# Kernel optimization log

Hardware: AMD Instinct MI355X
Metric: run time of the kernel (lower is better)

The kernel has to match this reference:

```python
import jax, jax.numpy as jnp
import numpy as np
import math

B, NB, HID, KD, NH = 256, 16, 512, 64, 8

def setup_inputs() -> dict:
    key = jax.random.key(0)
    ks = jax.random.split(key, 6)
    s = lambda fan_in: 1.0 / math.sqrt(fan_in)
    return {
        "h": jax.random.normal(ks[0], (B, NB, HID), dtype=jnp.float32),
        "mask": jax.random.randint(ks[1], (B, NB), 0, 2, dtype=jnp.int32),
        "Wk": jax.random.normal(ks[2], (NB, HID, KD * NH), dtype=jnp.float32) * s(HID),
        "Wq": jax.random.normal(ks[3], (NB, HID, KD * NH), dtype=jnp.float32) * s(HID),
        "Wv": jax.random.normal(ks[4], (NB, HID, HID * NH), dtype=jnp.float32) * s(HID),
        "Wo": jax.random.normal(ks[5], (NB, HID * NH, HID), dtype=jnp.float32) * s(HID * NH),
    }

def _group_linear(x, w):
    # x: (B, NB, din), w: (NB, din, dout) -> (B, NB, dout)
    return jnp.einsum('bnd,nde->bne', x, w)

def reference(h, mask, Wk, Wq, Wv, Wo):
    # grouped QKV projections
    k = _group_linear(h, Wk).reshape(B, NB, NH, KD).transpose(0, 2, 1, 3)    # (B,H,NB,KD)
    q = _group_linear(h, Wq).reshape(B, NB, NH, KD).transpose(0, 2, 1, 3)    # (B,H,NB,KD)
    v = _group_linear(h, Wv).reshape(B, NB, NH, HID).transpose(0, 2, 1, 3)   # (B,H,NB,HID)
    scores = jnp.einsum('bhqd,bhkd->bhqk', q, k) / math.sqrt(KD)             # (B,H,NB,NB)
    probs = jax.nn.softmax(scores, axis=-1)
    # post-softmax row mask: mask (B,NB) -> (B,1,NB,1)
    probs = probs * mask.astype(probs.dtype)[:, None, :, None]
    ctx = jnp.einsum('bhqk,bhkd->bhqd', probs, v)                            # (B,H,NB,HID)
    ctx = ctx.transpose(0, 2, 1, 3).reshape(B, NB, NH * HID)                 # (B,NB,H*HID)
    return _group_linear(ctx, Wo)                                            # (B,NB,HID)
```

## Files before the change

kernel.cpp:

```cpp
#include <hip/hip_runtime.h>


typedef short s16x4 __attribute__((ext_vector_type(4)));
typedef short s16x8 __attribute__((ext_vector_type(8)));
typedef float f32x4 __attribute__((ext_vector_type(4)));

__device__ __forceinline__ unsigned short f2bf(float f) {
  unsigned int u = __builtin_bit_cast(unsigned int, f);
  u += 0x7fffu + ((u >> 16) & 1u);
  return (unsigned short)(u >> 16);
}
__device__ __forceinline__ float bf2f(unsigned short s) {
  unsigned int u = ((unsigned int)s) << 16;
  return __builtin_bit_cast(float, u);
}

__global__ __launch_bounds__(256) void cvt_h(const float* __restrict__ h,
                                             unsigned short* __restrict__ hb)
{
  int i = (blockIdx.x * 256 + threadIdx.x) * 4;
  float4 v = *reinterpret_cast<const float4*>(h + i);
  s16x4 st = { (short)f2bf(v.x), (short)f2bf(v.y), (short)f2bf(v.z), (short)f2bf(v.w) };
  *reinterpret_cast<s16x4*>(hb + i) = st;
}

__global__ __launch_bounds__(256) void qkv_gemm(
    const unsigned short* __restrict__ hb, const float* __restrict__ Wq,
    const float* __restrict__ Wk, const float* __restrict__ Wv,
    unsigned short* __restrict__ qo, unsigned short* __restrict__ ko,
    unsigned short* __restrict__ vo)
{
  const int g    = blockIdx.y;
  const int n0   = blockIdx.x * 64;
  const int tid  = threadIdx.x;
  const int lane = tid & 63;
  const int wave = tid >> 6;
  const int wm   = wave * 64;

  const float* W; unsigned short* out; size_t obase; int oldc, wN, c0;
  if (n0 < 512)       { W = Wq + (size_t)g * 262144;  out = qo; obase = (size_t)g * 512;  oldc = 8192;  wN = 512;  c0 = n0; }
  else if (n0 < 1024) { W = Wk + (size_t)g * 262144;  out = ko; obase = (size_t)g * 512;  oldc = 8192;  wN = 512;  c0 = n0 - 512; }
  else                { W = Wv + (size_t)g * 2097152; out = vo; obase = (size_t)g * 4096; oldc = 65536; wN = 4096; c0 = n0 - 1024; }

  const unsigned short* A = hb + (size_t)g * 512;

  __shared__ unsigned short As[256][32];
  __shared__ unsigned short Bs[64][36];

  f32x4 acc[4][4];
  #pragma unroll
  for (int i = 0; i < 4; i++)
    #pragma unroll
    for (int j = 0; j < 4; j++) acc[i][j] = (f32x4){0.f, 0.f, 0.f, 0.f};

  const int fr = lane & 15, fq = lane >> 4;

  for (int k0 = 0; k0 < 512; k0 += 32) {
    __syncthreads();
    #pragma unroll
    for (int p = 0; p < 4; p++) {
      int idx = p * 256 + tid;
      int row = idx >> 2, kq = idx & 3;
      *reinterpret_cast<s16x8*>(&As[row][kq * 8]) =
          *reinterpret_cast<const s16x8*>(A + (size_t)row * 8192 + k0 + kq * 8);
    }
    #pragma unroll
    for (int p = 0; p < 2; p++) {
      int idx = p * 256 + tid;
      int n = idx & 63, kc = idx >> 6;
      const float* wp = W + (size_t)(k0 + kc * 4) * wN + c0 + n;
      float w0 = wp[0], w1 = wp[wN], w2 = wp[2 * wN], w3 = wp[3 * wN];
      s16x4 st = { (short)f2bf(w0), (short)f2bf(w1), (short)f2bf(w2), (short)f2bf(w3) };
      *reinterpret_cast<s16x4*>(&Bs[n][kc * 4]) = st;
    }
    __syncthreads();
    s16x8 af[4], bfr[4];
    #pragma unroll
    for (int mi = 0; mi < 4; mi++)
      af[mi] = *reinterpret_cast<const s16x8*>(&As[wm + mi * 16 + fr][fq * 8]);
    #pragma unroll
    for (int ni = 0; ni < 4; ni++) {
      const s16x4* bp = reinterpret_cast<const s16x4*>(&Bs[ni * 16 + fr][fq * 8]);
      s16x4 lo = bp[0], hi = bp[1];
      bfr[ni] = __builtin_shufflevector(lo, hi, 0, 1, 2, 3, 4, 5, 6, 7);
    }
    #pragma unroll
    for (int mi = 0; mi < 4; mi++)
      #pragma unroll
      for (int ni = 0; ni < 4; ni++)
        acc[mi][ni] = __builtin_amdgcn_mfma_f32_16x16x32_bf16(af[mi], bfr[ni], acc[mi][ni], 0, 0, 0);
  }

  #pragma unroll
  for (int mi = 0; mi < 4; mi++)
    #pragma unroll
    for (int ni = 0; ni < 4; ni++)
      #pragma unroll
      for (int r = 0; r < 4; r++) {
        int row = wm + mi * 16 + fq * 4 + r;
        int col = c0 + ni * 16 + fr;
        out[obase + (size_t)row * oldc + col] = f2bf(acc[mi][ni][r]);
      }
}

__global__ __launch_bounds__(256) void attn_kernel(
    const unsigned short* __restrict__ q, const unsigned short* __restrict__ k,
    const unsigned short* __restrict__ v, const int* __restrict__ mask,
    unsigned short* __restrict__ ctx)
{
  const int b  = blockIdx.x >> 3;
  const int hh = blockIdx.x & 7;
  const int tid = threadIdx.x;

  __shared__ float qs[16][65];
  __shared__ float ks[16][65];
  __shared__ float sc[16][16];

  {
    int n = tid >> 4, d4 = (tid & 15) * 4;
    size_t gi = ((size_t)(b * 16 + n) << 9) + (hh << 6) + d4;
    ushort4 qv = *reinterpret_cast<const ushort4*>(q + gi);
    ushort4 kv = *reinterpret_cast<const ushort4*>(k + gi);
    qs[n][d4] = bf2f(qv.x); qs[n][d4+1] = bf2f(qv.y); qs[n][d4+2] = bf2f(qv.z); qs[n][d4+3] = bf2f(qv.w);
    ks[n][d4] = bf2f(kv.x); ks[n][d4+1] = bf2f(kv.y); ks[n][d4+2] = bf2f(kv.z); ks[n][d4+3] = bf2f(kv.w);
  }
  __syncthreads();
  {
    int qi = tid >> 4, ki = tid & 15;
    float s = 0.f;
    #pragma unroll
    for (int j = 0; j < 64; j++) s += qs[qi][j] * ks[ki][j];
    sc[qi][ki] = s * 0.125f;
  }
  __syncthreads();
  if (tid < 16) {
    float m = sc[tid][0];
    #pragma unroll
    for (int j = 1; j < 16; j++) m = fmaxf(m, sc[tid][j]);
    float ev[16], sum = 0.f;
    #pragma unroll
    for (int j = 0; j < 16; j++) { ev[j] = __expf(sc[tid][j] - m); sum += ev[j]; }
    float scale = (mask[b * 16 + tid] != 0) ? (1.f / sum) : 0.f;
    #pragma unroll
    for (int j = 0; j < 16; j++) sc[tid][j] = ev[j] * scale;
  }
  __syncthreads();
  {
    int col4  = (tid & 127) * 4;
    int qbase = (tid >> 7) * 8;
    float a0[8], a1[8], a2[8], a3[8];
    #pragma unroll
    for (int j = 0; j < 8; j++) { a0[j] = 0.f; a1[j] = 0.f; a2[j] = 0.f; a3[j] = 0.f; }
    #pragma unroll
    for (int kk = 0; kk < 16; kk++) {
      ushort4 vv = *reinterpret_cast<const ushort4*>(
          v + ((size_t)(b * 16 + kk) << 12) + (hh << 9) + col4);
      float v0 = bf2f(vv.x), v1 = bf2f(vv.y), v2 = bf2f(vv.z), v3 = bf2f(vv.w);
      #pragma unroll
      for (int j = 0; j < 8; j++) {
        float p = sc[qbase + j][kk];
        a0[j] += p * v0; a1[j] += p * v1; a2[j] += p * v2; a3[j] += p * v3;
      }
    }
    #pragma unroll
    for (int j = 0; j < 8; j++) {
      ushort4 st = { f2bf(a0[j]), f2bf(a1[j]), f2bf(a2[j]), f2bf(a3[j]) };
      *reinterpret_cast<ushort4*>(
          ctx + ((size_t)(b * 16 + qbase + j) << 12) + (hh << 9) + col4) = st;
    }
  }
}

__global__ __launch_bounds__(512) void out_gemm(
    const unsigned short* __restrict__ ctxp, const float* __restrict__ Wo,
    float* __restrict__ partial)
{
  const int g    = blockIdx.y;
  const int bx   = blockIdx.x;
  const int sk   = bx >> 3;
  const int n0   = (bx & 7) * 64;
  const int tid  = threadIdx.x;
  const int lane = tid & 63;
  const int wave = tid >> 6;
  const int wm   = (wave >> 1) * 64;
  const int wn   = (wave & 1) * 32;

  const unsigned short* A = ctxp + (size_t)g * 4096;
  const float* W = Wo + (size_t)g * 2097152;

  __shared__ unsigned short As[256][32];
  __shared__ unsigned short Bs[64][36];

  f32x4 acc[4][2];
  #pragma unroll
  for (int i = 0; i < 4; i++)
    #pragma unroll
    for (int j = 0; j < 2; j++) acc[i][j] = (f32x4){0.f, 0.f, 0.f, 0.f};

  const int fr = lane & 15, fq = lane >> 4;
  const int kend = sk * 1024 + 1024;

  for (int k0 = sk * 1024; k0 < kend; k0 += 32) {
    __syncthreads();
    #pragma unroll
    for (int p = 0; p < 2; p++) {
      int idx = p * 512 + tid;
      int row = idx >> 2, kq = idx & 3;
      *reinterpret_cast<s16x8*>(&As[row][kq * 8]) =
          *reinterpret_cast<const s16x8*>(A + (size_t)row * 65536 + k0 + kq * 8);
    }
    {
      int n = tid & 63, kc = tid >> 6;
      const float* wp = W + (size_t)(k0 + kc * 4) * 512 + n0 + n;
      float w0 = wp[0], w1 = wp[512], w2 = wp[1024], w3 = wp[1536];
      s16x4 st = { (short)f2bf(w0), (short)f2bf(w1), (short)f2bf(w2), (short)f2bf(w3) };
      *reinterpret_cast<s16x4*>(&Bs[n][kc * 4]) = st;
    }
    __syncthreads();
    s16x8 af[4], bfr[2];
    #pragma unroll
    for (int mi = 0; mi < 4; mi++)
      af[mi] = *reinterpret_cast<const s16x8*>(&As[wm + mi * 16 + fr][fq * 8]);
    #pragma unroll
    for (int ni = 0; ni < 2; ni++) {
      const s16x4* bp = reinterpret_cast<const s16x4*>(&Bs[wn + ni * 16 + fr][fq * 8]);
      s16x4 lo = bp[0], hi = bp[1];
      bfr[ni] = __builtin_shufflevector(lo, hi, 0, 1, 2, 3, 4, 5, 6, 7);
    }
    #pragma unroll
    for (int mi = 0; mi < 4; mi++)
      #pragma unroll
      for (int ni = 0; ni < 2; ni++)
        acc[mi][ni] = __builtin_amdgcn_mfma_f32_16x16x32_bf16(af[mi], bfr[ni], acc[mi][ni], 0, 0, 0);
  }

  float* pg = partial + (size_t)sk * 2097152 + (size_t)g * 512;
  #pragma unroll
  for (int mi = 0; mi < 4; mi++)
    #pragma unroll
    for (int ni = 0; ni < 2; ni++)
      #pragma unroll
      for (int r = 0; r < 4; r++) {
        int row = wm + mi * 16 + fq * 4 + r;
        int col = n0 + wn + ni * 16 + fr;
        pg[(size_t)row * 8192 + col] = acc[mi][ni][r];
      }
}

__global__ __launch_bounds__(256) void reduce4(const float* __restrict__ part,
                                               float* __restrict__ out)
{
  int i = (blockIdx.x * 256 + threadIdx.x) * 4;
  float4 a = *reinterpret_cast<const float4*>(part + i);
  float4 b = *reinterpret_cast<const float4*>(part + 2097152 + i);
  float4 c = *reinterpret_cast<const float4*>(part + 4194304 + i);
  float4 d = *reinterpret_cast<const float4*>(part + 6291456 + i);
  float4 s = { a.x + b.x + c.x + d.x, a.y + b.y + c.y + d.y,
               a.z + b.z + c.z + d.z, a.w + b.w + c.w + d.w };
  *reinterpret_cast<float4*>(out + i) = s;
}

extern "C" void kernel_launch(void* const* d_in, const int* in_sizes, int n_in,
                              void* d_out, int out_size, void* d_ws, size_t ws_size,
                              hipStream_t stream) {
  const float* h  = (const float*)d_in[0];
  const int* mask = (const int*)d_in[1];
  const float* Wk = (const float*)d_in[2];
  const float* Wq = (const float*)d_in[3];
  const float* Wv = (const float*)d_in[4];
  const float* Wo = (const float*)d_in[5];
  float* out = (float*)d_out;

  unsigned short* qws   = (unsigned short*)d_ws;
  unsigned short* kws   = qws + 2097152;
  unsigned short* vws   = kws + 2097152;
  unsigned short* ctxws = vws + 16777216;
  unsigned short* hb    = ctxws;
  float* part           = (float*)d_ws;

  cvt_h<<<2048, 256, 0, stream>>>(h, hb);
  qkv_gemm<<<dim3(80, 16), 256, 0, stream>>>(hb, Wq, Wk, Wv, qws, kws, vws);
  attn_kernel<<<2048, 256, 0, stream>>>(qws, kws, vws, mask, ctxws);
  out_gemm<<<dim3(32, 16), 512, 0, stream>>>(ctxws, Wo, part);
  reduce4<<<2048, 256, 0, stream>>>(part, out);
}
```

Measured before the change: 388.0 us.

## Software-pipeline global loads into registers in QKV and output GEMMs

Result: slower. 672.5 us (+73.3%).

```diff
diff --git a/kernel.cpp b/kernel.cpp
--- a/kernel.cpp
+++ b/kernel.cpp
@@ -24,7 +24,7 @@
   *reinterpret_cast<s16x4*>(hb + i) = st;
 }
 
-__global__ __launch_bounds__(256) void qkv_gemm(
+__global__ __launch_bounds__(256, 4) void qkv_gemm(
     const unsigned short* __restrict__ hb, const float* __restrict__ Wq,
     const float* __restrict__ Wk, const float* __restrict__ Wv,
     unsigned short* __restrict__ qo, unsigned short* __restrict__ ko,
@@ -44,7 +44,7 @@
 
   const unsigned short* A = hb + (size_t)g * 512;
 
-  __shared__ unsigned short As[256][32];
+  __shared__ unsigned short As[256][40];
   __shared__ unsigned short Bs[64][36];
 
   f32x4 acc[4][4];
@@ -54,26 +54,55 @@
     for (int j = 0; j < 4; j++) acc[i][j] = (f32x4){0.f, 0.f, 0.f, 0.f};
 
   const int fr = lane & 15, fq = lane >> 4;
-
-  for (int k0 = 0; k0 < 512; k0 += 32) {
-    __syncthreads();
-    #pragma unroll
-    for (int p = 0; p < 4; p++) {
-      int idx = p * 256 + tid;
-      int row = idx >> 2, kq = idx & 3;
-      *reinterpret_cast<s16x8*>(&As[row][kq * 8]) =
-          *reinterpret_cast<const s16x8*>(A + (size_t)row * 8192 + k0 + kq * 8);
-    }
+  const int arow = tid >> 2, akq = tid & 3;
+  const int bn = tid & 63, bkc = tid >> 6;
+
+  s16x8 aR0[4], aR1[4];
+  f32x4 bR0[2], bR1[2];
+
+  auto LOAD0 = [&](int k0) {
+    #pragma unroll
+    for (int p = 0; p < 4; p++)
+      aR0[p] = *reinterpret_cast<const s16x8*>(A + (size_t)(p * 64 + arow) * 8192 + k0 + akq * 8);
     #pragma unroll
     for (int p = 0; p < 2; p++) {
-      int idx = p * 256 + tid;
-      int n = idx & 63, kc = idx >> 6;
-      const float* wp = W + (size_t)(k0 + kc * 4) * wN + c0 + n;
-      float w0 = wp[0], w1 = wp[wN], w2 = wp[2 * wN], w3 = wp[3 * wN];
-      s16x4 st = { (short)f2bf(w0), (short)f2bf(w1), (short)f2bf(w2), (short)f2bf(w3) };
-      *reinterpret_cast<s16x4*>(&Bs[n][kc * 4]) = st;
-    }
-    __syncthreads();
+      const float* wp = W + (size_t)(k0 + (p * 4 + bkc) * 4) * wN + c0 + bn;
+      bR0[p] = (f32x4){ wp[0], wp[wN], wp[2 * wN], wp[3 * wN] };
+    }
+  };
+  auto LOAD1 = [&](int k0) {
+    #pragma unroll
+    for (int p = 0; p < 4; p++)
+      aR1[p] = *reinterpret_cast<const s16x8*>(A + (size_t)(p * 64 + arow) * 8192 + k0 + akq * 8);
+    #pragma unroll
+    for (int p = 0; p < 2; p++) {
+      const float* wp = W + (size_t)(k0 + (p * 4 + bkc) * 4) * wN + c0 + bn;
+      bR1[p] = (f32x4){ wp[0], wp[wN], wp[2 * wN], wp[3 * wN] };
+    }
+  };
+  auto STORE0 = [&]() {
+    #pragma unroll
+    for (int p = 0; p < 4; p++)
+      *reinterpret_cast<s16x8*>(&As[p * 64 + arow][akq * 8]) = aR0[p];
+    #pragma unroll
+    for (int p = 0; p < 2; p++) {
+      s16x4 st = { (short)f2bf(bR0[p][0]), (short)f2bf(bR0[p][1]),
+                   (short)f2bf(bR0[p][2]), (short)f2bf(bR0[p][3]) };
+      *reinterpret_cast<s16x4*>(&Bs[bn][(p * 4 + bkc) * 4]) = st;
+    }
+  };
+  auto STORE1 = [&]() {
+    #pragma unroll
+    for (int p = 0; p < 4; p++)
+      *reinterpret_cast<s16x8*>(&As[p * 64 + arow][akq * 8]) = aR1[p];
+    #pragma unroll
+    for (int p = 0; p < 2; p++) {
+      s16x4 st = { (short)f2bf(bR1[p][0]), (short)f2bf(bR1[p][1]),
+                   (short)f2bf(bR1[p][2]), (short)f2bf(bR1[p][3]) };
+      *reinterpret_cast<s16x4*>(&Bs[bn][(p * 4 + bkc) * 4]) = st;
+    }
+  };
+  auto COMPUTE = [&]() {
     s16x8 af[4], bfr[4];
     #pragma unroll
     for (int mi = 0; mi < 4; mi++)
@@ -89,6 +118,26 @@
       #pragma unroll
       for (int ni = 0; ni < 4; ni++)
         acc[mi][ni] = __builtin_amdgcn_mfma_f32_16x16x32_bf16(af[mi], bfr[ni], acc[mi][ni], 0, 0, 0);
+  };
+
+  LOAD0(0);
+  LOAD1(32);
+  STORE0();
+  __syncthreads();
+
+  for (int k0 = 0; k0 < 512; k0 += 64) {
+    if (k0 + 64 < 512) LOAD0(k0 + 64);
+    COMPUTE();
+    __syncthreads();
+    STORE1();
+    __syncthreads();
+    if (k0 + 96 < 512) LOAD1(k0 + 96);
+    COMPUTE();
+    if (k0 + 64 < 512) {
+      __syncthreads();
+      STORE0();
+      __syncthreads();
+    }
   }
 
   #pragma unroll
@@ -171,7 +220,7 @@
   }
 }
 
-__global__ __launch_bounds__(512) void out_gemm(
+__global__ __launch_bounds__(512, 4) void out_gemm(
     const unsigned short* __restrict__ ctxp, const float* __restrict__ Wo,
     float* __restrict__ partial)
 {
@@ -188,7 +237,7 @@
   const unsigned short* A = ctxp + (size_t)g * 4096;
   const float* W = Wo + (size_t)g * 2097152;
 
-  __shared__ unsigned short As[256][32];
+  __shared__ unsigned short As[256][40];
   __shared__ unsigned short Bs[64][36];
 
   f32x4 acc[4][2];
@@ -198,25 +247,43 @@
     for (int j = 0; j < 2; j++) acc[i][j] = (f32x4){0.f, 0.f, 0.f, 0.f};
 
   const int fr = lane & 15, fq = lane >> 4;
-  const int kend = sk * 1024 + 1024;
-
-  for (int k0 = sk * 1024; k0 < kend; k0 += 32) {
-    __syncthreads();
-    #pragma unroll
-    for (int p = 0; p < 2; p++) {
-      int idx = p * 512 + tid;
-      int row = idx >> 2, kq = idx & 3;
-      *reinterpret_cast<s16x8*>(&As[row][kq * 8]) =
-          *reinterpret_cast<const s16x8*>(A + (size_t)row * 65536 + k0 + kq * 8);
-    }
-    {
-      int n = tid & 63, kc = tid >> 6;
-      const float* wp = W + (size_t)(k0 + kc * 4) * 512 + n0 + n;
-      float w0 = wp[0], w1 = wp[512], w2 = wp[1024], w3 = wp[1536];
-      s16x4 st = { (short)f2bf(w0), (short)f2bf(w1), (short)f2bf(w2), (short)f2bf(w3) };
-      *reinterpret_cast<s16x4*>(&Bs[n][kc * 4]) = st;
-    }
-    __syncthreads();
+  const int arow = tid >> 2, akq = tid & 3;
+  const int bn = tid & 63, bkc = tid >> 6;
+
+  s16x8 aR0[2], aR1[2];
+  f32x4 bR0, bR1;
+
+  auto LOAD0 = [&](int k0) {
+    #pragma unroll
+    for (int p = 0; p < 2; p++)
+      aR0[p] = *reinterpret_cast<const s16x8*>(A + (size_t)(p * 128 + arow) * 65536 + k0 + akq * 8);
+    const float* wp = W + (size_t)(k0 + bkc * 4) * 512 + n0 + bn;
+    bR0 = (f32x4){ wp[0], wp[512], wp[1024], wp[1536] };
+  };
+  auto LOAD1 = [&](int k0) {
+    #pragma unroll
+    for (int p = 0; p < 2; p++)
+      aR1[p] = *reinterpret_cast<const s16x8*>(A + (size_t)(p * 128 + arow) * 65536 + k0 + akq * 8);
+    const float* wp = W + (size_t)(k0 + bkc * 4) * 512 + n0 + bn;
+    bR1 = (f32x4){ wp[0], wp[512], wp[1024], wp[1536] };
+  };
+  auto STORE0 = [&]() {
+    #pragma unroll
+    for (int p = 0; p < 2; p++)
+      *reinterpret_cast<s16x8*>(&As[p * 128 + arow][akq * 8]) = aR0[p];
+    s16x4 st = { (short)f2bf(bR0[0]), (short)f2bf(bR0[1]),
+                 (short)f2bf(bR0[2]), (short)f2bf(bR0[3]) };
+    *reinterpret_cast<s16x4*>(&Bs[bn][bkc * 4]) = st;
+  };
+  auto STORE1 = [&]() {
+    #pragma unroll
+    for (int p = 0; p < 2; p++)
+      *reinterpret_cast<s16x8*>(&As[p * 128 + arow][akq * 8]) = aR1[p];
+    s16x4 st = { (short)f2bf(bR1[0]), (short)f2bf(bR1[1]),
+                 (short)f2bf(bR1[2]), (short)f2bf(bR1[3]) };
+    *reinterpret_cast<s16x4*>(&Bs[bn][bkc * 4]) = st;
+  };
+  auto COMPUTE = [&]() {
     s16x8 af[4], bfr[2];
     #pragma unroll
     for (int mi = 0; mi < 4; mi++)
@@ -232,6 +299,28 @@
       #pragma unroll
       for (int ni = 0; ni < 2; ni++)
         acc[mi][ni] = __builtin_amdgcn_mfma_f32_16x16x32_bf16(af[mi], bfr[ni], acc[mi][ni], 0, 0, 0);
+  };
+
+  const int ks = sk * 1024, kend = ks + 1024;
+
+  LOAD0(ks);
+  LOAD1(ks + 32);
+  STORE0();
+  __syncthreads();
+
+  for (int k0 = ks; k0 < kend; k0 += 64) {
+    if (k0 + 64 < kend) LOAD0(k0 + 64);
+    COMPUTE();
+    __syncthreads();
+    STORE1();
+    __syncthreads();
+    if (k0 + 96 < kend) LOAD1(k0 + 96);
+    COMPUTE();
+    if (k0 + 64 < kend) {
+      __syncthreads();
+      STORE0();
+      __syncthreads();
+    }
   }
 
   float* pg = partial + (size_t)sk * 2097152 + (size_t)g * 512;
```

## Register-prefetch next K tile and pad A shared tile in QKV/out GEMMs

Applied to the files above, without the earlier changes.

After: 387.4 us. About the same (-0.1%).

```diff
diff --git a/kernel.cpp b/kernel.cpp
--- a/kernel.cpp
+++ b/kernel.cpp
@@ -44,7 +44,7 @@
 
   const unsigned short* A = hb + (size_t)g * 512;
 
-  __shared__ unsigned short As[256][32];
+  __shared__ unsigned short As[256][40];
   __shared__ unsigned short Bs[64][36];
 
   f32x4 acc[4][4];
@@ -54,26 +54,34 @@
     for (int j = 0; j < 4; j++) acc[i][j] = (f32x4){0.f, 0.f, 0.f, 0.f};
 
   const int fr = lane & 15, fq = lane >> 4;
-
-  for (int k0 = 0; k0 < 512; k0 += 32) {
-    __syncthreads();
-    #pragma unroll
-    for (int p = 0; p < 4; p++) {
-      int idx = p * 256 + tid;
-      int row = idx >> 2, kq = idx & 3;
-      *reinterpret_cast<s16x8*>(&As[row][kq * 8]) =
-          *reinterpret_cast<const s16x8*>(A + (size_t)row * 8192 + k0 + kq * 8);
-    }
+  const int arow = tid >> 2, akq = tid & 3;
+  const int bn = tid & 63, bkc = tid >> 6;
+
+  s16x8 aR[4];
+  f32x4 bR[2];
+
+  auto LOAD = [&](int k0) {
+    #pragma unroll
+    for (int p = 0; p < 4; p++)
+      aR[p] = *reinterpret_cast<const s16x8*>(A + (size_t)(p * 64 + arow) * 8192 + k0 + akq * 8);
     #pragma unroll
     for (int p = 0; p < 2; p++) {
-      int idx = p * 256 + tid;
-      int n = idx & 63, kc = idx >> 6;
-      const float* wp = W + (size_t)(k0 + kc * 4) * wN + c0 + n;
-      float w0 = wp[0], w1 = wp[wN], w2 = wp[2 * wN], w3 = wp[3 * wN];
-      s16x4 st = { (short)f2bf(w0), (short)f2bf(w1), (short)f2bf(w2), (short)f2bf(w3) };
-      *reinterpret_cast<s16x4*>(&Bs[n][kc * 4]) = st;
-    }
-    __syncthreads();
+      const float* wp = W + (size_t)(k0 + (p * 4 + bkc) * 4) * wN + c0 + bn;
+      bR[p] = (f32x4){ wp[0], wp[wN], wp[2 * wN], wp[3 * wN] };
+    }
+  };
+  auto STORE = [&]() {
+    #pragma unroll
+    for (int p = 0; p < 4; p++)
+      *reinterpret_cast<s16x8*>(&As[p * 64 + arow][akq * 8]) = aR[p];
+    #pragma unroll
+    for (int p = 0; p < 2; p++) {
+      s16x4 st = { (short)f2bf(bR[p][0]), (short)f2bf(bR[p][1]),
+                   (short)f2bf(bR[p][2]), (short)f2bf(bR[p][3]) };
+      *reinterpret_cast<s16x4*>(&Bs[bn][(p * 4 + bkc) * 4]) = st;
+    }
+  };
+  auto COMPUTE = [&]() {
     s16x8 af[4], bfr[4];
     #pragma unroll
     for (int mi = 0; mi < 4; mi++)
@@ -89,6 +97,15 @@
       #pragma unroll
       for (int ni = 0; ni < 4; ni++)
         acc[mi][ni] = __builtin_amdgcn_mfma_f32_16x16x32_bf16(af[mi], bfr[ni], acc[mi][ni], 0, 0, 0);
+  };
+
+  LOAD(0);
+  for (int k0 = 0; k0 < 512; k0 += 32) {
+    __syncthreads();
+    STORE();
+    __syncthreads();
+    if (k0 + 32 < 512) LOAD(k0 + 32);
+    COMPUTE();
   }
 
   #pragma unroll
@@ -188,7 +205,7 @@
   const unsigned short* A = ctxp + (size_t)g * 4096;
   const float* W = Wo + (size_t)g * 2097152;
 
-  __shared__ unsigned short As[256][32];
+  __shared__ unsigned short As[256][40];
   __shared__ unsigned short Bs[64][36];
 
   f32x4 acc[4][2];
@@ -198,25 +215,28 @@
     for (int j = 0; j < 2; j++) acc[i][j] = (f32x4){0.f, 0.f, 0.f, 0.f};
 
   const int fr = lane & 15, fq = lane >> 4;
-  const int kend = sk * 1024 + 1024;
-
-  for (int k0 = sk * 1024; k0 < kend; k0 += 32) {
-    __syncthreads();
-    #pragma unroll
-    for (int p = 0; p < 2; p++) {
-      int idx = p * 512 + tid;
-      int row = idx >> 2, kq = idx & 3;
-      *reinterpret_cast<s16x8*>(&As[row][kq * 8]) =
-          *reinterpret_cast<const s16x8*>(A + (size_t)row * 65536 + k0 + kq * 8);
-    }
-    {
-      int n = tid & 63, kc = tid >> 6;
-      const float* wp = W + (size_t)(k0 + kc * 4) * 512 + n0 + n;
-      float w0 = wp[0], w1 = wp[512], w2 = wp[1024], w3 = wp[1536];
-      s16x4 st = { (short)f2bf(w0), (short)f2bf(w1), (short)f2bf(w2), (short)f2bf(w3) };
-      *reinterpret_cast<s16x4*>(&Bs[n][kc * 4]) = st;
-    }
-    __syncthreads();
+  const int arow = tid >> 2, akq = tid & 3;
+  const int bn = tid & 63, bkc = tid >> 6;
+
+  s16x8 aR[2];
+  f32x4 bR;
+
+  auto LOAD = [&](int k0) {
+    #pragma unroll
+    for (int p = 0; p < 2; p++)
+      aR[p] = *reinterpret_cast<const s16x8*>(A + (size_t)(p * 128 + arow) * 65536 + k0 + akq * 8);
+    const float* wp = W + (size_t)(k0 + bkc * 4) * 512 + n0 + bn;
+    bR = (f32x4){ wp[0], wp[512], wp[1024], wp[1536] };
+  };
+  auto STORE = [&]() {
+    #pragma unroll
+    for (int p = 0; p < 2; p++)
+      *reinterpret_cast<s16x8*>(&As[p * 128 + arow][akq * 8]) = aR[p];
+    s16x4 st = { (short)f2bf(bR[0]), (short)f2bf(bR[1]),
+                 (short)f2bf(bR[2]), (short)f2bf(bR[3]) };
+    *reinterpret_cast<s16x4*>(&Bs[bn][bkc * 4]) = st;
+  };
+  auto COMPUTE = [&]() {
     s16x8 af[4], bfr[2];
     #pragma unroll
     for (int mi = 0; mi < 4; mi++)
@@ -232,6 +252,17 @@
       #pragma unroll
       for (int ni = 0; ni < 2; ni++)
         acc[mi][ni] = __builtin_amdgcn_mfma_f32_16x16x32_bf16(af[mi], bfr[ni], acc[mi][ni], 0, 0, 0);
+  };
+
+  const int ks = sk * 1024, kend = ks + 1024;
+
+  LOAD(ks);
+  for (int k0 = ks; k0 < kend; k0 += 32) {
+    __syncthreads();
+    STORE();
+    __syncthreads();
+    if (k0 + 32 < kend) LOAD(k0 + 32);
+    COMPUTE();
   }
 
   float* pg = partial + (size_t)sk * 2097152 + (size_t)g * 512;
```

## Triple-buffer GEMM tiles with direct global-to-LDS loads in QKV and output GEMMs

Applied to the files above, without the earlier changes.

After: 392.9 us. About the same (+1.3%).

```diff
diff --git a/kernel.cpp b/kernel.cpp
--- a/kernel.cpp
+++ b/kernel.cpp
@@ -15,6 +15,12 @@
   return __builtin_bit_cast(float, u);
 }
 
+__device__ __forceinline__ void dma16(const void* g, void* l) {
+  __builtin_amdgcn_global_load_lds(
+      (const __attribute__((address_space(1))) void*)g,
+      (__attribute__((address_space(3))) void*)l, 16, 0, 0);
+}
+
 __global__ __launch_bounds__(256) void cvt_h(const float* __restrict__ h,
                                              unsigned short* __restrict__ hb)
 {
@@ -24,7 +30,7 @@
   *reinterpret_cast<s16x4*>(hb + i) = st;
 }
 
-__global__ __launch_bounds__(256) void qkv_gemm(
+__global__ __launch_bounds__(512) void qkv_gemm(
     const unsigned short* __restrict__ hb, const float* __restrict__ Wq,
     const float* __restrict__ Wk, const float* __restrict__ Wv,
     unsigned short* __restrict__ qo, unsigned short* __restrict__ ko,
@@ -35,7 +41,8 @@
   const int tid  = threadIdx.x;
   const int lane = tid & 63;
   const int wave = tid >> 6;
-  const int wm   = wave * 64;
+  const int wm   = (wave >> 1) * 64;
+  const int wn   = (wave & 1) * 32;
 
   const float* W; unsigned short* out; size_t obase; int oldc, wN, c0;
   if (n0 < 512)       { W = Wq + (size_t)g * 262144;  out = qo; obase = (size_t)g * 512;  oldc = 8192;  wN = 512;  c0 = n0; }
@@ -44,61 +51,64 @@
 
   const unsigned short* A = hb + (size_t)g * 512;
 
-  __shared__ unsigned short As[256][32];
-  __shared__ unsigned short Bs[64][36];
-
-  f32x4 acc[4][4];
+  __shared__ __align__(16) unsigned short As[3][256][32];
+  __shared__ __align__(16) float          Bs[3][32][64];
+
+  f32x4 acc[4][2];
   #pragma unroll
   for (int i = 0; i < 4; i++)
     #pragma unroll
-    for (int j = 0; j < 4; j++) acc[i][j] = (f32x4){0.f, 0.f, 0.f, 0.f};
+    for (int j = 0; j < 2; j++) acc[i][j] = (f32x4){0.f, 0.f, 0.f, 0.f};
 
   const int fr = lane & 15, fq = lane >> 4;
 
-  for (int k0 = 0; k0 < 512; k0 += 32) {
-    __syncthreads();
-    #pragma unroll
-    for (int p = 0; p < 4; p++) {
-      int idx = p * 256 + tid;
-      int row = idx >> 2, kq = idx & 3;
-      *reinterpret_cast<s16x8*>(&As[row][kq * 8]) =
-          *reinterpret_cast<const s16x8*>(A + (size_t)row * 8192 + k0 + kq * 8);
+  auto STAGE = [&](int buf, int k0) {
+    #pragma unroll
+    for (int p = 0; p < 2; p++)
+      dma16(A + (size_t)(p * 128 + (tid >> 2)) * 8192 + k0 + (tid & 3) * 8,
+            (char*)(&As[buf][0][0]) + p * 8192 + (size_t)tid * 16);
+    dma16(W + (size_t)(k0 + (tid >> 4)) * wN + c0 + (tid & 15) * 4,
+          (char*)(&Bs[buf][0][0]) + (size_t)tid * 16);
+  };
+
+  auto COMPUTE = [&](int buf) {
+    s16x8 af[4], bfr[2];
+    #pragma unroll
+    for (int mi = 0; mi < 4; mi++)
+      af[mi] = *reinterpret_cast<const s16x8*>(&As[buf][wm + mi * 16 + fr][fq * 8]);
+    #pragma unroll
+    for (int ni = 0; ni < 2; ni++) {
+      s16x8 bb;
+      #pragma unroll
+      for (int j = 0; j < 8; j++)
+        bb[j] = (short)f2bf(Bs[buf][fq * 8 + j][wn + ni * 16 + fr]);
+      bfr[ni] = bb;
     }
     #pragma unroll
-    for (int p = 0; p < 2; p++) {
-      int idx = p * 256 + tid;
-      int n = idx & 63, kc = idx >> 6;
-      const float* wp = W + (size_t)(k0 + kc * 4) * wN + c0 + n;
-      float w0 = wp[0], w1 = wp[wN], w2 = wp[2 * wN], w3 = wp[3 * wN];
-      s16x4 st = { (short)f2bf(w0), (short)f2bf(w1), (short)f2bf(w2), (short)f2bf(w3) };
-      *reinterpret_cast<s16x4*>(&Bs[n][kc * 4]) = st;
-    }
-    __syncthreads();
-    s16x8 af[4], bfr[4];
-    #pragma unroll
     for (int mi = 0; mi < 4; mi++)
-      af[mi] = *reinterpret_cast<const s16x8*>(&As[wm + mi * 16 + fr][fq * 8]);
-    #pragma unroll
-    for (int ni = 0; ni < 4; ni++) {
-      const s16x4* bp = reinterpret_cast<const s16x4*>(&Bs[ni * 16 + fr][fq * 8]);
-      s16x4 lo = bp[0], hi = bp[1];
-      bfr[ni] = __builtin_shufflevector(lo, hi, 0, 1, 2, 3, 4, 5, 6, 7);
-    }
-    #pragma unroll
-    for (int mi = 0; mi < 4; mi++)
-      #pragma unroll
-      for (int ni = 0; ni < 4; ni++)
+      #pragma unroll
+      for (int ni = 0; ni < 2; ni++)
         acc[mi][ni] = __builtin_amdgcn_mfma_f32_16x16x32_bf16(af[mi], bfr[ni], acc[mi][ni], 0, 0, 0);
+  };
+
+  STAGE(0, 0);
+  STAGE(1, 32);
+  for (int t = 0; t < 16; ++t) {
+    if (t < 15) asm volatile("s_waitcnt vmcnt(3)" ::: "memory");
+    else        asm volatile("s_waitcnt vmcnt(0)" ::: "memory");
+    __builtin_amdgcn_s_barrier();
+    if (t + 2 < 16) STAGE((t + 2) % 3, (t + 2) * 32);
+    COMPUTE(t % 3);
   }
 
   #pragma unroll
   for (int mi = 0; mi < 4; mi++)
     #pragma unroll
-    for (int ni = 0; ni < 4; ni++)
+    for (int ni = 0; ni < 2; ni++)
       #pragma unroll
       for (int r = 0; r < 4; r++) {
         int row = wm + mi * 16 + fq * 4 + r;
-        int col = c0 + ni * 16 + fr;
+        int col = c0 + wn + ni * 16 + fr;
         out[obase + (size_t)row * oldc + col] = f2bf(acc[mi][ni][r]);
       }
 }
@@ -188,8 +198,8 @@
   const unsigned short* A = ctxp + (size_t)g * 4096;
   const float* W = Wo + (size_t)g * 2097152;
 
-  __shared__ unsigned short As[256][32];
-  __shared__ unsigned short Bs[64][36];
+  __shared__ __align__(16) unsigned short As[3][256][32];
+  __shared__ __align__(16) float          Bs[3][32][64];
 
   f32x4 acc[4][2];
   #pragma unroll
@@ -198,40 +208,46 @@
     for (int j = 0; j < 2; j++) acc[i][j] = (f32x4){0.f, 0.f, 0.f, 0.f};
 
   const int fr = lane & 15, fq = lane >> 4;
-  const int kend = sk * 1024 + 1024;
-
-  for (int k0 = sk * 1024; k0 < kend; k0 += 32) {
-    __syncthreads();
-    #pragma unroll
-    for (int p = 0; p < 2; p++) {
-      int idx = p * 512 + tid;
-      int row = idx >> 2, kq = idx & 3;
-      *reinterpret_cast<s16x8*>(&As[row][kq * 8]) =
-          *reinterpret_cast<const s16x8*>(A + (size_t)row * 65536 + k0 + kq * 8);
-    }
-    {
-      int n = tid & 63, kc = tid >> 6;
-      const float* wp = W + (size_t)(k0 + kc * 4) * 512 + n0 + n;
-      float w0 = wp[0], w1 = wp[512], w2 = wp[1024], w3 = wp[1536];
-      s16x4 st = { (short)f2bf(w0), (short)f2bf(w1), (short)f2bf(w2), (short)f2bf(w3) };
-      *reinterpret_cast<s16x4*>(&Bs[n][kc * 4]) = st;
-    }
-    __syncthreads();
+
+  auto STAGE = [&](int buf, int k0) {
+    #pragma unroll
+    for (int p = 0; p < 2; p++)
+      dma16(A + (size_t)(p * 128 + (tid >> 2)) * 65536 + k0 + (tid & 3) * 8,
+            (char*)(&As[buf][0][0]) + p * 8192 + (size_t)tid * 16);
+    dma16(W + (size_t)(k0 + (tid >> 4)) * 512 + n0 + (tid & 15) * 4,
+          (char*)(&Bs[buf][0][0]) + (size_t)tid * 16);
+  };
+
+  auto COMPUTE = [&](int buf) {
     s16x8 af[4], bfr[2];
     #pragma unroll
     for (int mi = 0; mi < 4; mi++)
-      af[mi] = *reinterpret_cast<const s16x8*>(&As[wm + mi * 16 + fr][fq * 8]);
+      af[mi] = *reinterpret_cast<const s16x8*>(&As[buf][wm + mi * 16 + fr][fq * 8]);
     #pragma unroll
     for (int ni = 0; ni < 2; ni++) {
-      const s16x4* bp = reinterpret_cast<const s16x4*>(&Bs[wn + ni * 16 + fr][fq * 8]);
-      s16x4 lo = bp[0], hi = bp[1];
-      bfr[ni] = __builtin_shufflevector(lo, hi, 0, 1, 2, 3, 4, 5, 6, 7);
+      s16x8 bb;
+      #pragma unroll
+      for (int j = 0; j < 8; j++)
+        bb[j] = (short)f2bf(Bs[buf][fq * 8 + j][wn + ni * 16 + fr]);
+      bfr[ni] = bb;
     }
     #pragma unroll
     for (int mi = 0; mi < 4; mi++)
       #pragma unroll
       for (int ni = 0; ni < 2; ni++)
         acc[mi][ni] = __builtin_amdgcn_mfma_f32_16x16x32_bf16(af[mi], bfr[ni], acc[mi][ni], 0, 0, 0);
+  };
+
+  const int ks = sk * 1024;
+
+  STAGE(0, ks);
+  STAGE(1, ks + 32);
+  for (int t = 0; t < 32; ++t) {
+    if (t < 31) asm volatile("s_waitcnt vmcnt(3)" ::: "memory");
+    else        asm volatile("s_waitcnt vmcnt(0)" ::: "memory");
+    __builtin_amdgcn_s_barrier();
+    if (t + 2 < 32) STAGE((t + 2) % 3, ks + (t + 2) * 32);
+    COMPUTE(t % 3);
   }
 
   float* pg = partial + (size_t)sk * 2097152 + (size_t)g * 512;
@@ -279,7 +295,7 @@
   float* part           = (float*)d_ws;
 
   cvt_h<<<2048, 256, 0, stream>>>(h, hb);
-  qkv_gemm<<<dim3(80, 16), 256, 0, stream>>>(hb, Wq, Wk, Wv, qws, kws, vws);
+  qkv_gemm<<<dim3(80, 16), 512, 0, stream>>>(hb, Wq, Wk, Wv, qws, kws, vws);
   attn_kernel<<<2048, 256, 0, stream>>>(qws, kws, vws, mask, ctxws);
   out_gemm<<<dim3(32, 16), 512, 0, stream>>>(ctxws, Wo, part);
   reduce4<<<2048, 256, 0, stream>>>(part, out);
```
